# Kernel optimization log

Measured on AMD Instinct MI355X. Metric: run time of the kernel, lower is better.

The kernel has to match this reference:

```python
import jax, jax.numpy as jnp
import numpy as np

N_NODES = 100000
N_EDGES = 1600000
IN_FEATS = 128
HID = 32
N_REL = 5
N_BASES = 2
N_PAIRS = 4096


def setup_inputs() -> dict:
    key = jax.random.key(0)
    ks = jax.random.split(key, 24)
    d = {}
    d['x'] = jax.random.normal(ks[0], (N_NODES, IN_FEATS), dtype=jnp.float32)
    d['edge_mask'] = jnp.ones((N_EDGES,), dtype=jnp.float32)
    d['etype'] = jax.random.randint(ks[1], (N_EDGES,), 0, N_REL, dtype=jnp.int32)
    d['src'] = jax.random.randint(ks[2], (N_EDGES,), 0, N_NODES, dtype=jnp.int32)
    d['dst'] = jax.random.randint(ks[3], (N_EDGES,), 0, N_NODES, dtype=jnp.int32)
    d['users_idx'] = jax.random.randint(ks[4], (N_PAIRS,), 0, N_NODES, dtype=jnp.int32)
    d['items_idx'] = jax.random.randint(ks[5], (N_PAIRS,), 0, N_NODES, dtype=jnp.int32)
    # RelGraphConv params (basis decomposition): layer1 in->32, layers 2,3 32->32
    def s(k, din):
        return 1.0 / np.sqrt(din)
    d['V1'] = jax.random.normal(ks[6], (N_BASES, IN_FEATS, HID), dtype=jnp.float32) * s(0, IN_FEATS)
    d['comp1'] = jax.random.normal(ks[7], (N_REL, N_BASES), dtype=jnp.float32)
    d['loop1'] = jax.random.normal(ks[8], (IN_FEATS, HID), dtype=jnp.float32) * s(0, IN_FEATS)
    d['b1'] = jnp.zeros((HID,), dtype=jnp.float32)
    d['V2'] = jax.random.normal(ks[9], (N_BASES, HID, HID), dtype=jnp.float32) * s(0, HID)
    d['comp2'] = jax.random.normal(ks[10], (N_REL, N_BASES), dtype=jnp.float32)
    d['loop2'] = jax.random.normal(ks[11], (HID, HID), dtype=jnp.float32) * s(0, HID)
    d['b2'] = jnp.zeros((HID,), dtype=jnp.float32)
    d['V3'] = jax.random.normal(ks[12], (N_BASES, HID, HID), dtype=jnp.float32) * s(0, HID)
    d['comp3'] = jax.random.normal(ks[13], (N_REL, N_BASES), dtype=jnp.float32)
    d['loop3'] = jax.random.normal(ks[14], (HID, HID), dtype=jnp.float32) * s(0, HID)
    d['b3'] = jnp.zeros((HID,), dtype=jnp.float32)
    # MLP head: lin1 (2*sum(latent_dim[1:]) = 192 -> 128), lin2 (128 -> 1)
    d['w1'] = jax.random.normal(ks[15], (2 * 3 * HID, 128), dtype=jnp.float32) * (1.0 / np.sqrt(2 * 3 * HID))
    d['bw1'] = jnp.zeros((128,), dtype=jnp.float32)
    d['w2'] = jax.random.normal(ks[16], (128, 1), dtype=jnp.float32) * (1.0 / np.sqrt(128))
    d['bw2'] = jnp.zeros((1,), dtype=jnp.float32)
    return d


def _rgcn_layer(x, V, comp, loopw, bias, etype, src, dst, norm):
    # basis-decomposed relational conv: W_r = sum_b comp[r,b] * V[b]
    xb = jnp.einsum('nd,bdo->nbo', x, V)                       # [N,B,O]
    msg = jnp.einsum('eb,ebo->eo', comp[etype], xb[src])       # [E,O]
    msg = msg * norm[:, None]                                  # edge_mask norm
    agg = jax.ops.segment_sum(msg, dst, num_segments=x.shape[0])
    return jnp.tanh(agg + x @ loopw + bias)


def reference(x, edge_mask, etype, src, dst, users_idx, items_idx,
              V1, comp1, loop1, b1, V2, comp2, loop2, b2, V3, comp3, loop3, b3,
              w1, bw1, w2, bw2):
    h1 = _rgcn_layer(x, V1, comp1, loop1, b1, etype, src, dst, edge_mask)
    h2 = _rgcn_layer(h1, V2, comp2, loop2, b2, etype, src, dst, edge_mask)
    h3 = _rgcn_layer(h2, V3, comp3, loop3, b3, etype, src, dst, edge_mask)
    concat_states = jnp.concatenate([h1, h2, h3], axis=1)      # [N, 96]
    feats = jnp.concatenate([concat_states[users_idx], concat_states[items_idx]], axis=1)  # [P,192]
    hidden = jax.nn.relu(feats @ w1 + bw1)
    out = hidden @ w2 + bw2
    return out[:, 0]  # multiply_by = 1
```

## Files before the change

### kernel.cpp

```cpp
#include <hip/hip_runtime.h>
#include <stdint.h>

#define N_NODES  100000
#define N_EDGES  1600000
#define IN_FEATS 128
#define HID      32
#define N_REL    5
#define N_BASES  2
#define N_PAIRS  4096

#define NB        196
#define BCAP      16384
#define EPB       2048
#define SC_BLOCKS 782
#define TL1_BLOCKS 1250
#define NGROUPS   6250

typedef __attribute__((ext_vector_type(8))) short short8;
typedef __attribute__((ext_vector_type(4))) float f32x4;

__device__ inline unsigned int pack_bf16(float a, float b) {
    unsigned int ua = __float_as_uint(a), ub = __float_as_uint(b);
    ua = (ua + 0x7fffu + ((ua >> 16) & 1u)) >> 16;
    ub = (ub + 0x7fffu + ((ub >> 16) & 1u)) >> 16;
    return ua | (ub << 16);
}

__device__ inline unsigned short bf16_1(float a) {
    unsigned int u = __float_as_uint(a);
    u = (u + 0x7fffu + ((u >> 16) & 1u)) >> 16;
    return (unsigned short)u;
}


__global__ __launch_bounds__(256) void k_wprep(
    const float* __restrict__ V1, const float* __restrict__ comp1, const float* __restrict__ loop1,
    const float* __restrict__ V2, const float* __restrict__ comp2, const float* __restrict__ loop2,
    const float* __restrict__ V3, const float* __restrict__ comp3, const float* __restrict__ loop3,
    unsigned short* __restrict__ Wbf1, unsigned short* __restrict__ Wbf2,
    unsigned short* __restrict__ Wbf3, int* __restrict__ gcur) {
    int b = blockIdx.x;
    int t = threadIdx.x;
    if (b == 0 && t < NB) gcur[t] = 0;
    const float *V, *comp, *loopw;
    unsigned short* Wbf;
    int D, idx;
    if (b < 96)      { V = V1; comp = comp1; loopw = loop1; Wbf = Wbf1; D = IN_FEATS; idx = b * 256 + t; }
    else if (b < 120){ V = V2; comp = comp2; loopw = loop2; Wbf = Wbf2; D = HID;      idx = (b - 96) * 256 + t; }
    else             { V = V3; comp = comp3; loopw = loop3; Wbf = Wbf3; D = HID;      idx = (b - 120) * 256 + t; }
    if (idx >= 192 * D) return;
    int j = idx / D, k = idx % D;
    float v;
    if (j < 160) {
        int r = j >> 5, o = j & 31;
        v = comp[r * 2 + 0] * V[(size_t)(0 * D + k) * 32 + o]
          + comp[r * 2 + 1] * V[(size_t)(1 * D + k) * 32 + o];
    } else {
        v = loopw[k * 32 + (j - 160)];
    }
    Wbf[idx] = bf16_1(v);
}


__global__ __launch_bounds__(256) void k_fused1(
    const int* __restrict__ src, const int* __restrict__ dst,
    const int* __restrict__ etype, const float* __restrict__ mask,
    int* __restrict__ gcur, int2* __restrict__ ebuf,
    const float* __restrict__ xin,
    const unsigned short* __restrict__ Wbf, const float* __restrict__ bias,
    unsigned short* __restrict__ xs16, float* __restrict__ aggout) {
    int b = blockIdx.x;
    int t = threadIdx.x;
    if (b < SC_BLOCKS) {
        __shared__ int lh[NB];
        __shared__ int lex[NB];
        __shared__ int gbase[NB];
        __shared__ int scanbuf[256];
        __shared__ int2  srec[EPB];
        __shared__ short sb[EPB];
        int e0 = b * EPB;
        if (t < NB) lh[t] = 0;
        __syncthreads();
        int2 rec[8];
        int  bk[8];
#pragma unroll
        for (int i = 0; i < 8; i++) {
            int e = e0 + t + i * 256;
            if (e < N_EDGES) {
                int d = dst[e];
                bk[i] = d >> 9;
                rec[i].x = ((d & 511) << 23) | (src[e] * 80 + etype[e] * 16);
                rec[i].y = __float_as_int(mask[e]);
                atomicAdd(&lh[bk[i]], 1);
            } else bk[i] = -1;
        }
        __syncthreads();
        int cnt = (t < NB) ? lh[t] : 0;
        scanbuf[t] = cnt;
        __syncthreads();
        for (int off = 1; off < 256; off <<= 1) {
            int v = (t >= off) ? scanbuf[t - off] : 0;
            __syncthreads();
            scanbuf[t] += v;
            __syncthreads();
        }
        if (t < NB) {
            lex[t] = scanbuf[t] - cnt;
            gbase[t] = t * BCAP + (cnt ? atomicAdd(&gcur[t], cnt) : 0);
            lh[t] = 0;
        }
        __syncthreads();
#pragma unroll
        for (int i = 0; i < 8; i++) {
            if (bk[i] >= 0) {
                int p = lex[bk[i]] + atomicAdd(&lh[bk[i]], 1);
                srec[p] = rec[i];
                sb[p] = (short)bk[i];
            }
        }
        __syncthreads();
        int total = scanbuf[NB - 1];
        for (int idx = t; idx < total; idx += 256) {
            int bb = sb[idx];
            ebuf[gbase[bb] + (idx - lex[bb])] = srec[idx];
        }
        return;
    }
    __shared__ unsigned short As[16 * 136];
    int bb = b - SC_BLOCKS;
    int wv = t >> 6, lane = t & 63;
    int q = lane >> 4, n16 = lane & 15;
    short8 bfr[3][4];
#pragma unroll
    for (int i = 0; i < 3; i++) {
        int tt = wv * 3 + i;
#pragma unroll
        for (int ks = 0; ks < 4; ks++)
            bfr[i][ks] = *(const short8*)(Wbf + (tt * 16 + n16) * 128 + ks * 32 + q * 8);
    }
    float bv0 = bias[n16], bv1 = bias[16 + n16];
    int node_l = t >> 4;
    int seg    = t & 15;
    int g0 = bb * 5;
    float4 p0, p1;
    {
        const float* xr = xin + ((size_t)(g0 * 16 + node_l)) * 128 + seg * 8;
        p0 = *(const float4*)xr;
        p1 = *(const float4*)(xr + 4);
    }
    for (int gi = 0; gi < 5; gi++) {
        int g = g0 + gi;
        int n0 = g * 16;
        __syncthreads();
        {
            unsigned int u0 = pack_bf16(p0.x, p0.y);
            unsigned int u1 = pack_bf16(p0.z, p0.w);
            unsigned int u2 = pack_bf16(p1.x, p1.y);
            unsigned int u3 = pack_bf16(p1.z, p1.w);
            uint4 v; v.x = u0; v.y = u1; v.z = u2; v.w = u3;
            *(uint4*)(As + node_l * 136 + seg * 8) = v;
        }
        __syncthreads();
        if (gi + 1 < 5) {
            const float* xr = xin + ((size_t)((g + 1) * 16 + node_l)) * 128 + seg * 8;
            p0 = *(const float4*)xr;
            p1 = *(const float4*)(xr + 4);
        }
        short8 afr[4];
#pragma unroll
        for (int ks = 0; ks < 4; ks++)
            afr[ks] = *(const short8*)(As + n16 * 136 + ks * 32 + q * 8);
        f32x4 d[3];
        f32x4 z = {0.f, 0.f, 0.f, 0.f};
#pragma unroll
        for (int i = 0; i < 3; i++) d[i] = z;
#pragma unroll
        for (int i = 0; i < 3; i++)
#pragma unroll
            for (int ks = 0; ks < 4; ks++)
                d[i] = __builtin_amdgcn_mfma_f32_16x16x32_bf16(afr[ks], bfr[i][ks], d[i], 0, 0, 0);
#pragma unroll
        for (int i = 0; i < 3; i++) {
            int tt = wv * 3 + i;
            if (tt < 10) {
#pragma unroll
                for (int r = 0; r < 4; r++) {
                    int node = n0 + q * 4 + r;
                    xs16[(size_t)node * 160 + tt * 16 + n16] = bf16_1(d[i][r]);
                }
            } else {
                float bv = (tt == 10) ? bv0 : bv1;
                int o = (tt - 10) * 16 + n16;
#pragma unroll
                for (int r = 0; r < 4; r++) {
                    int node = n0 + q * 4 + r;
                    aggout[(size_t)node * 32 + o] = d[i][r] + bv;
                }
            }
        }
    }
}


__global__ __launch_bounds__(512) void k_bsort2(
    const int* __restrict__ gcur, const int2* __restrict__ ebuf,
    int2* __restrict__ esort, int* __restrict__ offsets) {
    __shared__ int hist[512];
    __shared__ int incl[512];
    __shared__ int cur[512];
    __shared__ int bs[256];
    __shared__ int sBase, sCnt;
    int blk = blockIdx.x, b = blk >> 1, h = blk & 1, t = threadIdx.x;
    if (t < 256) bs[t] = (t < NB) ? gcur[t] : 0;
    __syncthreads();
    for (int off = 1; off < 256; off <<= 1) {
        int v = 0;
        if (t < 256 && t >= off) v = bs[t - off];
        __syncthreads();
        if (t < 256) bs[t] += v;
        __syncthreads();
    }
    if (t == 0) { sCnt = gcur[b]; sBase = bs[b] - gcur[b]; }
    hist[t] = 0;
    __syncthreads();
    int cnt = sCnt, gbase = sBase;
    const int2* slab = ebuf + (size_t)b * BCAP;
    for (int e = t; e < cnt; e += 512) {
        int dl = ((unsigned)slab[e].x) >> 23;
        atomicAdd(&hist[dl], 1);
    }
    __syncthreads();
    incl[t] = hist[t];
    __syncthreads();
    for (int off = 1; off < 512; off <<= 1) {
        int v = 0;
        if (t >= off) v = incl[t - off];
        __syncthreads();
        incl[t] += v;
        __syncthreads();
    }
    int ex = incl[t] - hist[t];
    cur[t] = ex;
    if ((t >> 8) == h) {
        int n = (b << 9) + t;
        if (n <= N_NODES) offsets[n] = gbase + ex;
    }
    if (b == NB - 1 && h == 1 && t == 0) offsets[N_NODES] = N_EDGES;
    __syncthreads();
    for (int e = t; e < cnt; e += 512) {
        int2 pk = slab[e];
        int dl = ((unsigned)pk.x) >> 23;
        if ((dl >> 8) == h) {
            int pos = gbase + atomicAdd(&cur[dl], 1);
            int2 rec;
            rec.x = pk.x & 0x7fffff;
            rec.y = pk.y;
            esort[pos] = rec;
        }
    }
}


__global__ __launch_bounds__(256) void k_agg_t(
    const int* __restrict__ offsets, const int2* __restrict__ esort,
    const unsigned int* __restrict__ xrel16, const float* __restrict__ agg,
    float* __restrict__ hout, int hoff,
    const unsigned short* __restrict__ Wbf, const float* __restrict__ bias,
    unsigned short* __restrict__ xs16_out, float* __restrict__ agg_out) {
    __shared__ unsigned int hbf[32][20];
    int t = threadIdx.x;
    int nl = t >> 3;
    int v = blockIdx.x * 32 + nl;
    int o = t & 7;
    int s0 = offsets[v], s1 = offsets[v + 1];
    float4 a0 = *(const float4*)(agg + (size_t)v * 32 + o * 4);
    float acc0 = a0.x, acc1 = a0.y, acc2 = a0.z, acc3 = a0.w;
    int last = s1 - 1;
    for (int e = s0; e < s1; e += 16) {
        int addr[16];
        float m[16];
#pragma unroll
        for (int i = 0; i < 16; i++) {
            int ei = e + i;
            int ec = (ei <= last) ? ei : last;
            int2 pk = esort[ec];
            addr[i] = pk.x;
            m[i] = (ei <= last) ? __int_as_float(pk.y) : 0.f;
        }
        uint2 xw[16];
#pragma unroll
        for (int i = 0; i < 16; i++)
            xw[i] = *(const uint2*)(xrel16 + (unsigned)addr[i] + o * 2);
#pragma unroll
        for (int i = 0; i < 16; i++) {
            float f0 = __uint_as_float(xw[i].x << 16);
            float f1 = __uint_as_float(xw[i].x & 0xffff0000u);
            float f2 = __uint_as_float(xw[i].y << 16);
            float f3 = __uint_as_float(xw[i].y & 0xffff0000u);
            acc0 = fmaf(m[i], f0, acc0);
            acc1 = fmaf(m[i], f1, acc1);
            acc2 = fmaf(m[i], f2, acc2);
            acc3 = fmaf(m[i], f3, acc3);
        }
    }
    float4 r;
    r.x = tanhf(acc0); r.y = tanhf(acc1); r.z = tanhf(acc2); r.w = tanhf(acc3);
    *(float4*)(hout + (size_t)v * 96 + hoff + o * 4) = r;
    hbf[nl][o * 2]     = pack_bf16(r.x, r.y);
    hbf[nl][o * 2 + 1] = pack_bf16(r.z, r.w);
    __syncthreads();
    int wv = t >> 6, lane = t & 63;
    int q = lane >> 4, n16 = lane & 15;
    int gg = wv & 1;
    int tbase = (wv >> 1) * 6;
    short8 afr = *(const short8*)&hbf[gg * 16 + n16][q * 4];
    short8 bfr[6];
#pragma unroll
    for (int j = 0; j < 6; j++)
        bfr[j] = *(const short8*)(Wbf + ((tbase + j) * 16 + n16) * 32 + q * 8);
    f32x4 d[6];
    f32x4 z = {0.f, 0.f, 0.f, 0.f};
#pragma unroll
    for (int j = 0; j < 6; j++) d[j] = z;
#pragma unroll
    for (int j = 0; j < 6; j++)
        d[j] = __builtin_amdgcn_mfma_f32_16x16x32_bf16(afr, bfr[j], d[j], 0, 0, 0);
    float bv0 = bias[n16], bv1 = bias[16 + n16];
    int n0 = blockIdx.x * 32 + gg * 16;
#pragma unroll
    for (int j = 0; j < 6; j++) {
        int tt = tbase + j;
        if (tt < 10) {
#pragma unroll
            for (int rr = 0; rr < 4; rr++) {
                int node = n0 + q * 4 + rr;
                xs16_out[(size_t)node * 160 + tt * 16 + n16] = bf16_1(d[j][rr]);
            }
        } else {
            float bv = (tt == 10) ? bv0 : bv1;
            int oo = (tt - 10) * 16 + n16;
#pragma unroll
            for (int rr = 0; rr < 4; rr++) {
                int node = n0 + q * 4 + rr;
                agg_out[(size_t)node * 32 + oo] = d[j][rr] + bv;
            }
        }
    }
}


__global__ __launch_bounds__(256) void k_agg(
    const int* __restrict__ offsets, const int2* __restrict__ esort,
    const unsigned int* __restrict__ xrel16, const float* __restrict__ agg,
    float* __restrict__ hout, int hoff) {
    int v = blockIdx.x * 32 + (threadIdx.x >> 3);
    int o = threadIdx.x & 7;
    if (v >= N_NODES) return;
    int s0 = offsets[v], s1 = offsets[v + 1];
    float4 a0 = *(const float4*)(agg + (size_t)v * 32 + o * 4);
    float acc0 = a0.x, acc1 = a0.y, acc2 = a0.z, acc3 = a0.w;
    int last = s1 - 1;
    for (int e = s0; e < s1; e += 16) {
        int addr[16];
        float m[16];
#pragma unroll
        for (int i = 0; i < 16; i++) {
            int ei = e + i;
            int ec = (ei <= last) ? ei : last;
            int2 pk = esort[ec];
            addr[i] = pk.x;
            m[i] = (ei <= last) ? __int_as_float(pk.y) : 0.f;
        }
        uint2 xw[16];
#pragma unroll
        for (int i = 0; i < 16; i++)
            xw[i] = *(const uint2*)(xrel16 + (unsigned)addr[i] + o * 2);
#pragma unroll
        for (int i = 0; i < 16; i++) {
            float f0 = __uint_as_float(xw[i].x << 16);
            float f1 = __uint_as_float(xw[i].x & 0xffff0000u);
            float f2 = __uint_as_float(xw[i].y << 16);
            float f3 = __uint_as_float(xw[i].y & 0xffff0000u);
            acc0 = fmaf(m[i], f0, acc0);
            acc1 = fmaf(m[i], f1, acc1);
            acc2 = fmaf(m[i], f2, acc2);
            acc3 = fmaf(m[i], f3, acc3);
        }
    }
    float4 r;
    r.x = tanhf(acc0); r.y = tanhf(acc1); r.z = tanhf(acc2); r.w = tanhf(acc3);
    *(float4*)(hout + (size_t)v * 96 + hoff + o * 4) = r;
}


__global__ void k_mlp(const float* __restrict__ concat, const int* __restrict__ uidx,
                      const int* __restrict__ iidx,
                      const float* __restrict__ w1, const float* __restrict__ bw1,
                      const float* __restrict__ w2, const float* __restrict__ bw2,
                      float* __restrict__ out) {
    __shared__ float feats[192];
    __shared__ float red[2];
    int p = blockIdx.x;
    int t = threadIdx.x;
    int u = uidx[p], it = iidx[p];
    for (int k = t; k < 192; k += 128)
        feats[k] = (k < 96) ? concat[(size_t)u * 96 + k] : concat[(size_t)it * 96 + (k - 96)];
    __syncthreads();
    float acc = bw1[t];
    for (int k = 0; k < 192; k++) acc += feats[k] * w1[k * 128 + t];
    float h = fmaxf(acc, 0.f);
    float part = h * w2[t];
    for (int off = 32; off > 0; off >>= 1) part += __shfl_down(part, off, 64);
    if ((t & 63) == 0) red[t >> 6] = part;
    __syncthreads();
    if (t == 0) out[p] = red[0] + red[1] + bw2[0];
}


extern "C" void kernel_launch(void* const* d_in, const int* in_sizes, int n_in,
                              void* d_out, int out_size, void* d_ws, size_t ws_size,
                              hipStream_t stream) {
    const float* x         = (const float*)d_in[0];
    const float* edge_mask = (const float*)d_in[1];
    const int*   etype     = (const int*)d_in[2];
    const int*   src       = (const int*)d_in[3];
    const int*   dst       = (const int*)d_in[4];
    const int*   users_idx = (const int*)d_in[5];
    const int*   items_idx = (const int*)d_in[6];
    const float* V1        = (const float*)d_in[7];
    const float* comp1     = (const float*)d_in[8];
    const float* loop1     = (const float*)d_in[9];
    const float* b1        = (const float*)d_in[10];
    const float* V2        = (const float*)d_in[11];
    const float* comp2     = (const float*)d_in[12];
    const float* loop2     = (const float*)d_in[13];
    const float* b2        = (const float*)d_in[14];
    const float* V3        = (const float*)d_in[15];
    const float* comp3     = (const float*)d_in[16];
    const float* loop3     = (const float*)d_in[17];
    const float* b3        = (const float*)d_in[18];
    const float* w1        = (const float*)d_in[19];
    const float* bw1       = (const float*)d_in[20];
    const float* w2        = (const float*)d_in[21];
    const float* bw2       = (const float*)d_in[22];
    float* out = (float*)d_out;

    uintptr_t w = (uintptr_t)d_ws;
    auto al = [&](size_t bytes) { uintptr_t p = (w + 255) & ~(uintptr_t)255; w = p + bytes; return p; };
    int*   gcur    = (int*)al(sizeof(int) * NB);
    int*   offsets = (int*)al(sizeof(int) * (N_NODES + 1));
    int2*  ebuf    = (int2*)al(sizeof(int2) * (size_t)NB * BCAP);
    unsigned int* xrelA = (unsigned int*)al(sizeof(unsigned int) * (size_t)N_NODES * 80);
    unsigned int* xrelB = (unsigned int*)al(sizeof(unsigned int) * (size_t)N_NODES * 80);
    int2*  esort   = (int2*)al(sizeof(int2) * N_EDGES);
    unsigned short* Wbf1 = (unsigned short*)al(sizeof(unsigned short) * 192 * IN_FEATS);
    unsigned short* Wbf2 = (unsigned short*)al(sizeof(unsigned short) * 192 * HID);
    unsigned short* Wbf3 = (unsigned short*)al(sizeof(unsigned short) * 192 * HID);
    float* aggA    = (float*)al(sizeof(float) * (size_t)N_NODES * 32);
    float* aggB    = (float*)al(sizeof(float) * (size_t)N_NODES * 32);
    float* concat  = (float*)al(sizeof(float) * (size_t)N_NODES * 96);

    k_wprep<<<144, 256, 0, stream>>>(V1, comp1, loop1, V2, comp2, loop2,
                                     V3, comp3, loop3, Wbf1, Wbf2, Wbf3, gcur);
    k_fused1<<<SC_BLOCKS + TL1_BLOCKS, 256, 0, stream>>>(
        src, dst, etype, edge_mask, gcur, ebuf,
        x, Wbf1, b1, (unsigned short*)xrelA, aggA);
    k_bsort2<<<2 * NB, 512, 0, stream>>>(gcur, ebuf, esort, offsets);

    const int agrid = N_NODES / 32;

    k_agg_t<<<agrid, 256, 0, stream>>>(offsets, esort, xrelA, aggA, concat, 0,
                                       Wbf2, b2, (unsigned short*)xrelB, aggB);
    k_agg_t<<<agrid, 256, 0, stream>>>(offsets, esort, xrelB, aggB, concat, 32,
                                       Wbf3, b3, (unsigned short*)xrelA, aggA);
    k_agg<<<agrid, 256, 0, stream>>>(offsets, esort, xrelA, aggA, concat, 64);

    k_mlp<<<N_PAIRS, 128, 0, stream>>>(concat, users_idx, items_idx, w1, bw1, w2, bw2, out);
}
```

Measured before the change: 345.6 us.

## Aggregate raw hidden states per basis before transforming in layers two and three

After: 318.5 us. 7.8% less time.

```diff
diff --git a/kernel.cpp b/kernel.cpp
--- a/kernel.cpp
+++ b/kernel.cpp
@@ -32,33 +32,51 @@
     return (unsigned short)u;
 }
 
+__device__ inline void split_bf16_2(float a, float b, unsigned int& hi, unsigned int& lo) {
+    unsigned int ha = bf16_1(a), hb = bf16_1(b);
+    hi = ha | (hb << 16);
+    float fa = __uint_as_float(ha << 16), fb = __uint_as_float(hb << 16);
+    lo = pack_bf16(a - fa, b - fb);
+}
+
 
 __global__ __launch_bounds__(256) void k_wprep(
     const float* __restrict__ V1, const float* __restrict__ comp1, const float* __restrict__ loop1,
-    const float* __restrict__ V2, const float* __restrict__ comp2, const float* __restrict__ loop2,
-    const float* __restrict__ V3, const float* __restrict__ comp3, const float* __restrict__ loop3,
-    unsigned short* __restrict__ Wbf1, unsigned short* __restrict__ Wbf2,
-    unsigned short* __restrict__ Wbf3, int* __restrict__ gcur) {
+    const float* __restrict__ V2, const float* __restrict__ loop2,
+    const float* __restrict__ V3, const float* __restrict__ loop3,
+    unsigned short* __restrict__ Wbf1, unsigned short* __restrict__ Wcat2,
+    unsigned short* __restrict__ Wcat3, int* __restrict__ gcur) {
     int b = blockIdx.x;
     int t = threadIdx.x;
     if (b == 0 && t < NB) gcur[t] = 0;
-    const float *V, *comp, *loopw;
-    unsigned short* Wbf;
-    int D, idx;
-    if (b < 96)      { V = V1; comp = comp1; loopw = loop1; Wbf = Wbf1; D = IN_FEATS; idx = b * 256 + t; }
-    else if (b < 120){ V = V2; comp = comp2; loopw = loop2; Wbf = Wbf2; D = HID;      idx = (b - 96) * 256 + t; }
-    else             { V = V3; comp = comp3; loopw = loop3; Wbf = Wbf3; D = HID;      idx = (b - 120) * 256 + t; }
-    if (idx >= 192 * D) return;
-    int j = idx / D, k = idx % D;
+    if (b < 96) {
+        int idx = b * 256 + t;
+        if (idx >= 192 * IN_FEATS) return;
+        int j = idx / IN_FEATS, k = idx % IN_FEATS;
+        float v;
+        if (j < 160) {
+            int r = j >> 5, o = j & 31;
+            v = comp1[r * 2 + 0] * V1[(size_t)(0 * IN_FEATS + k) * 32 + o]
+              + comp1[r * 2 + 1] * V1[(size_t)(1 * IN_FEATS + k) * 32 + o];
+        } else {
+            v = loop1[k * 32 + (j - 160)];
+        }
+        Wbf1[idx] = bf16_1(v);
+        return;
+    }
+    const float *V, *loopw;
+    unsigned short* Wc;
+    int idx;
+    if (b < 116) { V = V2; loopw = loop2; Wc = Wcat2; idx = (b - 96) * 256 + t; }
+    else         { V = V3; loopw = loop3; Wc = Wcat3; idx = (b - 116) * 256 + t; }
+    if (idx >= 32 * 160) return;
+    int col = idx / 160, k = idx % 160;
+    int seg = k >> 5, inner = k & 31;
     float v;
-    if (j < 160) {
-        int r = j >> 5, o = j & 31;
-        v = comp[r * 2 + 0] * V[(size_t)(0 * D + k) * 32 + o]
-          + comp[r * 2 + 1] * V[(size_t)(1 * D + k) * 32 + o];
-    } else {
-        v = loopw[k * 32 + (j - 160)];
-    }
-    Wbf[idx] = bf16_1(v);
+    if (seg < 2)      v = V[inner * 32 + col];
+    else if (seg < 4) v = V[(32 + inner) * 32 + col];
+    else              v = loopw[inner * 32 + col];
+    Wc[idx] = bf16_1(v);
 }
 
 
@@ -89,7 +107,7 @@
             if (e < N_EDGES) {
                 int d = dst[e];
                 bk[i] = d >> 9;
-                rec[i].x = ((d & 511) << 23) | (src[e] * 80 + etype[e] * 16);
+                rec[i].x = ((d & 511) << 23) | (src[e] << 4) | etype[e];
                 rec[i].y = __float_as_int(mask[e]);
                 atomicAdd(&lh[bk[i]], 1);
             } else bk[i] = -1;
@@ -261,17 +279,12 @@
 }
 
 
-__global__ __launch_bounds__(256) void k_agg_t(
+__global__ __launch_bounds__(256) void k_agg1(
     const int* __restrict__ offsets, const int2* __restrict__ esort,
     const unsigned int* __restrict__ xrel16, const float* __restrict__ agg,
-    float* __restrict__ hout, int hoff,
-    const unsigned short* __restrict__ Wbf, const float* __restrict__ bias,
-    unsigned short* __restrict__ xs16_out, float* __restrict__ agg_out) {
-    __shared__ unsigned int hbf[32][20];
-    int t = threadIdx.x;
-    int nl = t >> 3;
-    int v = blockIdx.x * 32 + nl;
-    int o = t & 7;
+    float* __restrict__ concat, unsigned int* __restrict__ hrel_out) {
+    int v = blockIdx.x * 32 + (threadIdx.x >> 3);
+    int o = threadIdx.x & 7;
     int s0 = offsets[v], s1 = offsets[v + 1];
     float4 a0 = *(const float4*)(agg + (size_t)v * 32 + o * 4);
     float acc0 = a0.x, acc1 = a0.y, acc2 = a0.z, acc3 = a0.w;
@@ -284,7 +297,8 @@
             int ei = e + i;
             int ec = (ei <= last) ? ei : last;
             int2 pk = esort[ec];
-            addr[i] = pk.x;
+            int low = pk.x;
+            addr[i] = (low >> 4) * 80 + (low & 15) * 16;
             m[i] = (ei <= last) ? __int_as_float(pk.y) : 0.f;
         }
         uint2 xw[16];
@@ -305,91 +319,92 @@
     }
     float4 r;
     r.x = tanhf(acc0); r.y = tanhf(acc1); r.z = tanhf(acc2); r.w = tanhf(acc3);
-    *(float4*)(hout + (size_t)v * 96 + hoff + o * 4) = r;
-    hbf[nl][o * 2]     = pack_bf16(r.x, r.y);
-    hbf[nl][o * 2 + 1] = pack_bf16(r.z, r.w);
-    __syncthreads();
-    int wv = t >> 6, lane = t & 63;
-    int q = lane >> 4, n16 = lane & 15;
-    int gg = wv & 1;
-    int tbase = (wv >> 1) * 6;
-    short8 afr = *(const short8*)&hbf[gg * 16 + n16][q * 4];
-    short8 bfr[6];
-#pragma unroll
-    for (int j = 0; j < 6; j++)
-        bfr[j] = *(const short8*)(Wbf + ((tbase + j) * 16 + n16) * 32 + q * 8);
-    f32x4 d[6];
-    f32x4 z = {0.f, 0.f, 0.f, 0.f};
-#pragma unroll
-    for (int j = 0; j < 6; j++) d[j] = z;
-#pragma unroll
-    for (int j = 0; j < 6; j++)
-        d[j] = __builtin_amdgcn_mfma_f32_16x16x32_bf16(afr, bfr[j], d[j], 0, 0, 0);
-    float bv0 = bias[n16], bv1 = bias[16 + n16];
-    int n0 = blockIdx.x * 32 + gg * 16;
-#pragma unroll
-    for (int j = 0; j < 6; j++) {
-        int tt = tbase + j;
-        if (tt < 10) {
-#pragma unroll
-            for (int rr = 0; rr < 4; rr++) {
-                int node = n0 + q * 4 + rr;
-                xs16_out[(size_t)node * 160 + tt * 16 + n16] = bf16_1(d[j][rr]);
-            }
-        } else {
-            float bv = (tt == 10) ? bv0 : bv1;
-            int oo = (tt - 10) * 16 + n16;
-#pragma unroll
-            for (int rr = 0; rr < 4; rr++) {
-                int node = n0 + q * 4 + rr;
-                agg_out[(size_t)node * 32 + oo] = d[j][rr] + bv;
-            }
-        }
-    }
-}
-
-
-__global__ __launch_bounds__(256) void k_agg(
+    *(float4*)(concat + (size_t)v * 96 + o * 4) = r;
+    hrel_out[v * 16 + o * 2]     = pack_bf16(r.x, r.y);
+    hrel_out[v * 16 + o * 2 + 1] = pack_bf16(r.z, r.w);
+}
+
+
+__global__ __launch_bounds__(256) void k_agg23(
     const int* __restrict__ offsets, const int2* __restrict__ esort,
-    const unsigned int* __restrict__ xrel16, const float* __restrict__ agg,
-    float* __restrict__ hout, int hoff) {
-    int v = blockIdx.x * 32 + (threadIdx.x >> 3);
-    int o = threadIdx.x & 7;
-    if (v >= N_NODES) return;
+    const unsigned int* __restrict__ hrel_in, const float* __restrict__ comp,
+    const unsigned short* __restrict__ Wcat, const float* __restrict__ bias,
+    float* __restrict__ concat, int hoff, unsigned int* __restrict__ hrel_out) {
+    __shared__ unsigned int hbf[32][84];
+    __shared__ float2 cLds[5];
+    int t = threadIdx.x;
+    if (t < 5) cLds[t] = ((const float2*)comp)[t];
+    int nl = t >> 3;
+    int v = blockIdx.x * 32 + nl;
+    int o = t & 7;
     int s0 = offsets[v], s1 = offsets[v + 1];
-    float4 a0 = *(const float4*)(agg + (size_t)v * 32 + o * 4);
-    float acc0 = a0.x, acc1 = a0.y, acc2 = a0.z, acc3 = a0.w;
+    __syncthreads();
+    float y00 = 0.f, y01 = 0.f, y02 = 0.f, y03 = 0.f;
+    float y10 = 0.f, y11 = 0.f, y12 = 0.f, y13 = 0.f;
     int last = s1 - 1;
     for (int e = s0; e < s1; e += 16) {
         int addr[16];
-        float m[16];
+        float c0[16], c1[16];
 #pragma unroll
         for (int i = 0; i < 16; i++) {
             int ei = e + i;
             int ec = (ei <= last) ? ei : last;
             int2 pk = esort[ec];
-            addr[i] = pk.x;
-            m[i] = (ei <= last) ? __int_as_float(pk.y) : 0.f;
+            int low = pk.x;
+            addr[i] = low & 0x7ffff0;
+            float2 cc = cLds[low & 15];
+            float m = (ei <= last) ? __int_as_float(pk.y) : 0.f;
+            c0[i] = m * cc.x;
+            c1[i] = m * cc.y;
         }
         uint2 xw[16];
 #pragma unroll
         for (int i = 0; i < 16; i++)
-            xw[i] = *(const uint2*)(xrel16 + (unsigned)addr[i] + o * 2);
+            xw[i] = *(const uint2*)(hrel_in + (unsigned)addr[i] + o * 2);
 #pragma unroll
         for (int i = 0; i < 16; i++) {
             float f0 = __uint_as_float(xw[i].x << 16);
             float f1 = __uint_as_float(xw[i].x & 0xffff0000u);
             float f2 = __uint_as_float(xw[i].y << 16);
             float f3 = __uint_as_float(xw[i].y & 0xffff0000u);
-            acc0 = fmaf(m[i], f0, acc0);
-            acc1 = fmaf(m[i], f1, acc1);
-            acc2 = fmaf(m[i], f2, acc2);
-            acc3 = fmaf(m[i], f3, acc3);
-        }
-    }
-    float4 r;
-    r.x = tanhf(acc0); r.y = tanhf(acc1); r.z = tanhf(acc2); r.w = tanhf(acc3);
-    *(float4*)(hout + (size_t)v * 96 + hoff + o * 4) = r;
+            y00 = fmaf(c0[i], f0, y00); y10 = fmaf(c1[i], f0, y10);
+            y01 = fmaf(c0[i], f1, y01); y11 = fmaf(c1[i], f1, y11);
+            y02 = fmaf(c0[i], f2, y02); y12 = fmaf(c1[i], f2, y12);
+            y03 = fmaf(c0[i], f3, y03); y13 = fmaf(c1[i], f3, y13);
+        }
+    }
+    unsigned int hi, lo;
+    split_bf16_2(y00, y01, hi, lo);
+    hbf[nl][o * 2]          = hi;  hbf[nl][16 + o * 2]     = lo;
+    split_bf16_2(y02, y03, hi, lo);
+    hbf[nl][o * 2 + 1]      = hi;  hbf[nl][16 + o * 2 + 1] = lo;
+    split_bf16_2(y10, y11, hi, lo);
+    hbf[nl][32 + o * 2]     = hi;  hbf[nl][48 + o * 2]     = lo;
+    split_bf16_2(y12, y13, hi, lo);
+    hbf[nl][32 + o * 2 + 1] = hi;  hbf[nl][48 + o * 2 + 1] = lo;
+    *(uint2*)&hbf[nl][64 + o * 2] = *(const uint2*)(hrel_in + v * 16 + o * 2);
+    __syncthreads();
+    int wv = t >> 6, lane = t & 63;
+    int q = lane >> 4, n16 = lane & 15;
+    int gg = wv & 1;
+    int tt = wv >> 1;
+    f32x4 d = {0.f, 0.f, 0.f, 0.f};
+#pragma unroll
+    for (int ks = 0; ks < 5; ks++) {
+        short8 afr = *(const short8*)&hbf[gg * 16 + n16][ks * 16 + q * 4];
+        short8 bfr = *(const short8*)(Wcat + (tt * 16 + n16) * 160 + ks * 32 + q * 8);
+        d = __builtin_amdgcn_mfma_f32_16x16x32_bf16(afr, bfr, d, 0, 0, 0);
+    }
+    float bv = bias[tt * 16 + n16];
+    int n0 = blockIdx.x * 32 + gg * 16;
+#pragma unroll
+    for (int r = 0; r < 4; r++) {
+        int node = n0 + q * 4 + r;
+        float h = tanhf(d[r] + bv);
+        concat[(size_t)node * 96 + hoff + tt * 16 + n16] = h;
+        if (hrel_out)
+            ((unsigned short*)hrel_out)[node * 32 + tt * 16 + n16] = bf16_1(h);
+    }
 }
 
 
@@ -450,30 +465,30 @@
     int*   gcur    = (int*)al(sizeof(int) * NB);
     int*   offsets = (int*)al(sizeof(int) * (N_NODES + 1));
     int2*  ebuf    = (int2*)al(sizeof(int2) * (size_t)NB * BCAP);
-    unsigned int* xrelA = (unsigned int*)al(sizeof(unsigned int) * (size_t)N_NODES * 80);
-    unsigned int* xrelB = (unsigned int*)al(sizeof(unsigned int) * (size_t)N_NODES * 80);
+    unsigned int* xs16  = (unsigned int*)al(sizeof(unsigned int) * (size_t)N_NODES * 80);
+    unsigned int* hrel1 = (unsigned int*)al(sizeof(unsigned int) * (size_t)N_NODES * 16);
+    unsigned int* hrel2 = (unsigned int*)al(sizeof(unsigned int) * (size_t)N_NODES * 16);
     int2*  esort   = (int2*)al(sizeof(int2) * N_EDGES);
-    unsigned short* Wbf1 = (unsigned short*)al(sizeof(unsigned short) * 192 * IN_FEATS);
-    unsigned short* Wbf2 = (unsigned short*)al(sizeof(unsigned short) * 192 * HID);
-    unsigned short* Wbf3 = (unsigned short*)al(sizeof(unsigned short) * 192 * HID);
+    unsigned short* Wbf1  = (unsigned short*)al(sizeof(unsigned short) * 192 * IN_FEATS);
+    unsigned short* Wcat2 = (unsigned short*)al(sizeof(unsigned short) * 32 * 160);
+    unsigned short* Wcat3 = (unsigned short*)al(sizeof(unsigned short) * 32 * 160);
     float* aggA    = (float*)al(sizeof(float) * (size_t)N_NODES * 32);
-    float* aggB    = (float*)al(sizeof(float) * (size_t)N_NODES * 32);
     float* concat  = (float*)al(sizeof(float) * (size_t)N_NODES * 96);
 
-    k_wprep<<<144, 256, 0, stream>>>(V1, comp1, loop1, V2, comp2, loop2,
-                                     V3, comp3, loop3, Wbf1, Wbf2, Wbf3, gcur);
+    k_wprep<<<136, 256, 0, stream>>>(V1, comp1, loop1, V2, loop2, V3, loop3,
+                                     Wbf1, Wcat2, Wcat3, gcur);
     k_fused1<<<SC_BLOCKS + TL1_BLOCKS, 256, 0, stream>>>(
         src, dst, etype, edge_mask, gcur, ebuf,
-        x, Wbf1, b1, (unsigned short*)xrelA, aggA);
+        x, Wbf1, b1, (unsigned short*)xs16, aggA);
     k_bsort2<<<2 * NB, 512, 0, stream>>>(gcur, ebuf, esort, offsets);
 
     const int agrid = N_NODES / 32;
 
-    k_agg_t<<<agrid, 256, 0, stream>>>(offsets, esort, xrelA, aggA, concat, 0,
-                                       Wbf2, b2, (unsigned short*)xrelB, aggB);
-    k_agg_t<<<agrid, 256, 0, stream>>>(offsets, esort, xrelB, aggB, concat, 32,
-                                       Wbf3, b3, (unsigned short*)xrelA, aggA);
-    k_agg<<<agrid, 256, 0, stream>>>(offsets, esort, xrelA, aggA, concat, 64);
+    k_agg1<<<agrid, 256, 0, stream>>>(offsets, esort, xs16, aggA, concat, hrel1);
+    k_agg23<<<agrid, 256, 0, stream>>>(offsets, esort, hrel1, comp2, Wcat2, b2,
+                                       concat, 32, hrel2);
+    k_agg23<<<agrid, 256, 0, stream>>>(offsets, esort, hrel2, comp3, Wcat3, b3,
+                                       concat, 64, (unsigned int*)nullptr);
 
     k_mlp<<<N_PAIRS, 128, 0, stream>>>(concat, users_idx, items_idx, w1, bw1, w2, bw2, out);
 }
```
